# Kernel optimization log

Measured on AMD Instinct MI355X. Metric: run time of the kernel, lower is better.

Reference implementation:

```python
import jax, jax.numpy as jnp
import numpy as np

N, D, H, E, K = 16384, 256, 512, 16, 2  # nodes, node_dim, expert hidden, n_experts, active_k
LB_WEIGHT = 0.01
EPS = 1e-5


def setup_inputs() -> dict:
    key = jax.random.key(0)
    k0, k1, k2, k3 = jax.random.split(key, 4)
    x = jax.random.normal(k0, (N, D), jnp.float32)
    # router weight: torch nn.Linear(D, E, bias=False) -> weight [E, D], init std=0.02
    Wr = jax.random.normal(k1, (E, D), jnp.float32) * 0.02
    # stacked expert weights (torch Linear weights transposed to [in, out])
    W1 = jax.random.normal(k2, (E, D, H), jnp.float32) * 0.02
    W2 = jax.random.normal(k3, (E, H, D), jnp.float32) * 0.02
    ln_gamma = jnp.ones((D,), jnp.float32)
    ln_beta = jnp.zeros((D,), jnp.float32)
    return {"x": x, "Wr": Wr, "W1": W1, "W2": W2, "ln_gamma": ln_gamma, "ln_beta": ln_beta}


def reference(x, Wr, W1, W2, ln_gamma, ln_beta):
    n = x.shape[0]
    router_logits = x @ Wr.T                                  # [N, E]
    router_probs = jax.nn.softmax(router_logits, axis=-1)     # [N, E]
    top_w, top_i = jax.lax.top_k(router_probs, K)             # [N, K] each
    top_w = top_w / (top_w.sum(axis=-1, keepdims=True) + 1e-9)
    # dense combine weights: cw[n, e] = renormalized weight if e selected else 0
    cw = jnp.zeros((n, E), x.dtype).at[jnp.arange(n)[:, None], top_i].set(top_w)
    # per-expert FFN on all tokens (fixed-shape dense dispatch), exact-erf GELU like nn.GELU
    h = jax.nn.gelu(jnp.einsum('nd,edh->neh', x, W1), approximate=False)  # [N, E, H]
    y = jnp.einsum('neh,ehd->ned', h, W2)                     # [N, E, D]
    moe_out = jnp.einsum('ne,ned->nd', cw, y)                 # [N, D]
    # residual + LayerNorm
    z = x + moe_out
    mu = z.mean(axis=-1, keepdims=True)
    var = ((z - mu) ** 2).mean(axis=-1, keepdims=True)
    out = (z - mu) / jnp.sqrt(var + EPS) * ln_gamma + ln_beta
    # load-balance loss (counts are non-differentiable, like torch.no_grad())
    counts = jax.ops.segment_sum(jnp.ones((n * K,), router_probs.dtype),
                                 top_i.reshape(-1), num_segments=E)
    frac_tokens = jax.lax.stop_gradient(counts) / (n * K + 1e-9)
    lb_loss = LB_WEIGHT * (E * jnp.sum(frac_tokens * router_probs.mean(axis=0)))
    return out, lb_loss, jax.lax.stop_gradient(router_probs), top_i
```

## Files before the change

### kernel.cpp

```cpp
#include <hip/hip_runtime.h>
#include <hip/hip_bf16.h>
#include <math.h>

#define N_TOK 16384
#define DIM   256
#define HID   512
#define NEXP  16
#define NSLOT (N_TOK * 2)
#define RT    64
#define MAXT  (NSLOT / RT + NEXP)
#define XCDC  (MAXT / 8)

typedef __attribute__((ext_vector_type(8))) short bf16x8;
typedef __attribute__((ext_vector_type(4))) float f32x4;
#define MFMA(a, b, c) __builtin_amdgcn_mfma_f32_16x16x32_bf16(a, b, c, 0, 0, 0)

__device__ __forceinline__ unsigned short f2b(float f) {
  union { float f; unsigned int i; } c; c.f = f;
  unsigned int r = c.i + 0x7FFFu + ((c.i >> 16) & 1u);
  return (unsigned short)(r >> 16);
}

__device__ __forceinline__ float gelu_f(float v) {
  float v2 = v * v;
  float u2 = v * fmaf(0.10294322f, v2, 2.3022082f);
  float s  = __builtin_amdgcn_exp2f(u2);
  float r  = __builtin_amdgcn_rcpf(1.0f + s);
  return fmaf(-v, r, v);
}

__global__ __launch_bounds__(256) void prep_kernel(
    const float* __restrict__ W1, const float* __restrict__ W2,
    unsigned short* __restrict__ W1f, unsigned short* __restrict__ W2f)
{
  int id = blockIdx.x * 256 + threadIdx.x;
  if (id < 524288) {
    int i4 = id * 4;
    int inner = i4 & 31;
    int h  = (i4 >> 5) & 511;
    int kb = (i4 >> 14) & 7;
    int e  = i4 >> 17;
    const float* src = W1 + ((size_t)(e * 256 + kb * 32 + inner) * 512 + h);
    ushort4 o;
    o.x = f2b(src[0]); o.y = f2b(src[512]); o.z = f2b(src[1024]); o.w = f2b(src[1536]);
    *(ushort4*)(W1f + i4) = o;
  } else {
    int i4 = (id - 524288) * 4;
    int inner = i4 & 31;
    int d2 = (i4 >> 5) & 255;
    int kb = (i4 >> 13) & 15;
    int e  = i4 >> 17;
    const float* src = W2 + ((size_t)(e * 512 + kb * 32 + inner) * 256 + d2);
    ushort4 o;
    o.x = f2b(src[0]); o.y = f2b(src[256]); o.z = f2b(src[512]); o.w = f2b(src[768]);
    *(ushort4*)(W2f + i4) = o;
  }
}

__global__ __launch_bounds__(256) void router_kernel(
    const float* __restrict__ x, const float* __restrict__ Wr,
    float* __restrict__ probs_out, float* __restrict__ topi_out,
    float* __restrict__ topw, int* __restrict__ sel, float* __restrict__ g_partial,
    unsigned short* __restrict__ xb)
{
  __shared__ float sp[16];
  int tid = threadIdx.x;
  int wv = tid >> 6, lane = tid & 63;
  int tok = blockIdx.x * 4 + wv;
  int e = lane & 15, q = lane >> 4;
  if (tid < 16) sp[tid] = 0.f;
  __syncthreads();

  const float4* xr = (const float4*)(x + (size_t)tok * DIM + q * 64);
  const float4* wr = (const float4*)(Wr + (size_t)e * DIM + q * 64);
  float a0 = 0.f, a1 = 0.f, a2 = 0.f, a3 = 0.f;
  #pragma unroll
  for (int i = 0; i < 16; ++i) {
    float4 xa = xr[i], wa = wr[i];
    a0 += xa.x * wa.x; a1 += xa.y * wa.y; a2 += xa.z * wa.z; a3 += xa.w * wa.w;
  }
  float lg = (a0 + a1) + (a2 + a3);
  lg += __shfl_xor(lg, 16, 64);
  lg += __shfl_xor(lg, 32, 64);

  float mx = lg;
  #pragma unroll
  for (int o = 1; o < 16; o <<= 1) mx = fmaxf(mx, __shfl_xor(mx, o, 64));
  float ex = expf(lg - mx);
  float ssum = ex;
  #pragma unroll
  for (int o = 1; o < 16; o <<= 1) ssum += __shfl_xor(ssum, o, 64);
  float p = ex / ssum;

  if (lane < 16) {
    probs_out[(size_t)tok * NEXP + e] = p;
    atomicAdd(&sp[e], p);
  }

  {
    float4 xc = *(const float4*)(x + (size_t)tok * DIM + lane * 4);
    ushort4 o;
    o.x = f2b(xc.x); o.y = f2b(xc.y); o.z = f2b(xc.z); o.w = f2b(xc.w);
    *(ushort4*)(xb + (size_t)tok * DIM + lane * 4) = o;
  }

  float p1 = p; int i1 = e;
  #pragma unroll
  for (int o = 1; o < 16; o <<= 1) {
    float po = __shfl_xor(p1, o, 64); int io = __shfl_xor(i1, o, 64);
    if (po > p1 || (po == p1 && io < i1)) { p1 = po; i1 = io; }
  }
  float pm = (e == i1) ? -1.f : p;
  float p2 = pm; int i2 = e;
  #pragma unroll
  for (int o = 1; o < 16; o <<= 1) {
    float po = __shfl_xor(p2, o, 64); int io = __shfl_xor(i2, o, 64);
    if (po > p2 || (po == p2 && io < i2)) { p2 = po; i2 = io; }
  }
  if (lane == 0) {
    float rs = 1.0f / (p1 + p2 + 1e-9f);
    int s0 = tok * 2;
    topw[s0] = p1 * rs;  topw[s0 + 1] = p2 * rs;
    sel[s0] = i1;        sel[s0 + 1] = i2;
    topi_out[s0] = (float)i1;  topi_out[s0 + 1] = (float)i2;
  }
  __syncthreads();
  if (tid < 16) g_partial[(size_t)tid * 4096 + blockIdx.x] = sp[tid];
}

__global__ __launch_bounds__(256) void scatter_kernel(
    const int* __restrict__ sel, const float* __restrict__ topw,
    const float* __restrict__ g_partial,
    int* __restrict__ cursors, int* __restrict__ gdone,
    int* __restrict__ tok_of_pos, float* __restrict__ w_of_pos,
    float* __restrict__ zbuf, int* __restrict__ perm, float* __restrict__ lb_out)
{
  __shared__ int bcnt[16];
  __shared__ int bbase[16];
  int tid = threadIdx.x;
  if (tid < 16) bcnt[tid] = 0;
  __syncthreads();
  int s = blockIdx.x * 256 + tid;
  int e = sel[s];
  int my = atomicAdd(&bcnt[e], 1);
  __syncthreads();
  if (tid < 16) bbase[tid] = atomicAdd(&cursors[tid], bcnt[tid]);
  __syncthreads();
  int idx = e * NSLOT + bbase[e] + my;
  tok_of_pos[idx] = s >> 1;
  w_of_pos[idx]   = topw[s];

  {
    float4 zz = {0.f, 0.f, 0.f, 0.f};
    float4* zp = (float4*)zbuf + (size_t)blockIdx.x * 8192 + tid;
    #pragma unroll
    for (int i = 0; i < 32; ++i) zp[i * 256] = zz;
  }

  __threadfence();
  __shared__ int lastS;
  if (tid == 0) lastS = (atomicAdd(gdone, 1) == 127) ? 1 : 0;
  __syncthreads();
  if (!lastS) return;

  __shared__ float sp[16];
  __shared__ int nt[16];
  __shared__ int P[9];
  __shared__ int ccnt[16];
  int wv = tid >> 6, lane = tid & 63;
  if (tid < 16) ccnt[tid] = atomicAdd(&cursors[tid], 0);
  #pragma unroll
  for (int ee = 0; ee < 4; ++ee) {
    int ex = wv * 4 + ee;
    float sacc = 0.f;
    #pragma unroll
    for (int j = 0; j < 64; ++j) sacc += g_partial[(size_t)ex * 4096 + j * 64 + lane];
    #pragma unroll
    for (int o = 32; o; o >>= 1) sacc += __shfl_xor(sacc, o, 64);
    if (lane == 0) sp[ex] = sacc;
  }
  __syncthreads();
  if (tid < 16) nt[tid] = (ccnt[tid] + RT - 1) / RT;
  __syncthreads();
  if (tid == 0) {
    float acc = 0.f;
    for (int e2 = 0; e2 < NEXP; ++e2)
      acc += ((float)ccnt[e2] / (32768.0f + 1e-9f)) * (sp[e2] * (1.0f / 16384.0f));
    lb_out[0] = 0.01f * 16.0f * acc;
    int pp = 0;
    for (int g = 0; g < 8; ++g) { P[g] = pp; pp += nt[g] + nt[g + 8]; }
    P[8] = pp;
  }
  __syncthreads();
  for (int t = tid; t < MAXT; t += 256) {
    int g = 0;
    #pragma unroll
    for (int gg = 1; gg < 8; ++gg) if (t >= P[gg]) g = gg;
    int v = -1;
    if (t < P[8]) {
      int r = t - P[g];
      int e2 = (r < nt[g]) ? g : g + 8;
      int mt = (r < nt[g]) ? r : r - nt[g];
      v = (e2 << 16) | mt;
    }
    perm[t] = v;
  }
}

__global__ __launch_bounds__(512, 1) void ffn_kernel(
    const unsigned short* __restrict__ xb,
    const unsigned short* __restrict__ W1f, const unsigned short* __restrict__ W2f,
    const int* __restrict__ cursors, const int* __restrict__ perm,
    const int* __restrict__ tok_of_pos, const float* __restrict__ w_of_pos,
    float* __restrict__ zbuf)
{
  __shared__ __align__(16) unsigned short As[8 * 64 * 32];
  __shared__ __align__(16) unsigned short Hs[16 * 64 * 32];
  __shared__ float rwS[RT];
  __shared__ int   tokS[RT];

  int b = blockIdx.x;
  int rr = (b & 7) * XCDC + (b >> 3);
  int pv = perm[rr];
  if (pv < 0) return;
  int e = pv >> 16, mtile = pv & 0xFFFF;
  int cnt = cursors[e];
  int base = e * NSLOT;
  int m0 = mtile * RT;

  int tid = threadIdx.x;
  if (tid < RT) {
    int rl = m0 + tid;
    tokS[tid] = (rl < cnt) ? tok_of_pos[base + rl] : -1;
    rwS[tid]  = (rl < cnt) ? w_of_pos[base + rl] : 0.f;
  }
  __syncthreads();

  #pragma unroll
  for (int q = 0; q < 4; ++q) {
    int idx = q * 512 + tid;
    int row = idx >> 5, cb = idx & 31;
    int tk = tokS[row];
    bf16x8 v = {0, 0, 0, 0, 0, 0, 0, 0};
    if (tk >= 0) v = *(const bf16x8*)(xb + (size_t)tk * DIM + cb * 8);
    int si = ((cb >> 2) * 2048 + row * 32 + (cb & 3) * 8) ^ ((row & 7) << 3);
    *(bf16x8*)&As[si] = v;
  }
  __syncthreads();

  int lane = tid & 63;
  int w = tid >> 6;
  int l15 = lane & 15, g = lane >> 4;

  bf16x8 af[4][8];
  #pragma unroll
  for (int mf = 0; mf < 4; ++mf) {
    int row = mf * 16 + l15;
    #pragma unroll
    for (int kb = 0; kb < 8; ++kb)
      af[mf][kb] = *(const bf16x8*)&As[(kb * 2048 + row * 32 + g * 8) ^ ((row & 7) << 3)];
  }

  const unsigned short* W1e = W1f + (size_t)e * (8 * 512 * 32);
  #pragma unroll
  for (int cf = 0; cf < 4; ++cf) {
    int col0 = w * 64 + cf * 16;
    f32x4 ac[4];
    #pragma unroll
    for (int mf = 0; mf < 4; ++mf) ac[mf] = (f32x4){0.f, 0.f, 0.f, 0.f};
    #pragma unroll
    for (int kb = 0; kb < 8; ++kb) {
      bf16x8 bfr = *(const bf16x8*)(W1e + (size_t)(kb * 512 + col0 + l15) * 32 + g * 8);
      #pragma unroll
      for (int mf = 0; mf < 4; ++mf) ac[mf] = MFMA(af[mf][kb], bfr, ac[mf]);
    }
    int col = col0 + l15;
    #pragma unroll
    for (int mf = 0; mf < 4; ++mf) {
      #pragma unroll
      for (int reg = 0; reg < 4; ++reg) {
        int row = mf * 16 + g * 4 + reg;
        int si = ((col >> 5) * 2048 + row * 32 + (col & 31)) ^ ((row & 7) << 3);
        Hs[si] = f2b(gelu_f(ac[mf][reg]));
      }
    }
  }
  __syncthreads();

  const unsigned short* W2e = W2f + (size_t)e * (16 * 256 * 32);
  bf16x8 b2[2][16];
  #pragma unroll
  for (int cf = 0; cf < 2; ++cf)
    #pragma unroll
    for (int kb = 0; kb < 16; ++kb)
      b2[cf][kb] = *(const bf16x8*)(W2e + (size_t)(kb * 256 + w * 32 + cf * 16 + l15) * 32 + g * 8);

  #pragma unroll
  for (int mf = 0; mf < 4; ++mf) {
    f32x4 ac0 = {0.f, 0.f, 0.f, 0.f}, ac1 = {0.f, 0.f, 0.f, 0.f};
    int rowa = mf * 16 + l15;
    #pragma unroll
    for (int kb = 0; kb < 16; ++kb) {
      bf16x8 hfr = *(const bf16x8*)&Hs[(kb * 2048 + rowa * 32 + g * 8) ^ ((rowa & 7) << 3)];
      ac0 = MFMA(hfr, b2[0][kb], ac0);
      ac1 = MFMA(hfr, b2[1][kb], ac1);
    }
    #pragma unroll
    for (int reg = 0; reg < 4; ++reg) {
      int row = mf * 16 + g * 4 + reg;
      int t = tokS[row];
      if (t >= 0) {
        float rw = rwS[row];
        atomicAdd(zbuf + (size_t)t * DIM + w * 32 + l15,      ac0[reg] * rw);
        atomicAdd(zbuf + (size_t)t * DIM + w * 32 + 16 + l15, ac1[reg] * rw);
      }
    }
  }
}

__global__ __launch_bounds__(256) void combine_ln_kernel(
    const float* __restrict__ x, const float* __restrict__ zbuf,
    const float* __restrict__ gamma, const float* __restrict__ beta,
    float* __restrict__ outp)
{
  int wv = threadIdx.x >> 6, lane = threadIdx.x & 63;
  int tok = blockIdx.x * 4 + wv;
  int d0 = lane << 2;
  float4 xv = *(const float4*)(x + (size_t)tok * DIM + d0);
  float4 mv = *(const float4*)(zbuf + (size_t)tok * DIM + d0);
  float z0 = xv.x + mv.x, z1 = xv.y + mv.y, z2 = xv.z + mv.z, z3 = xv.w + mv.w;
  float s = z0 + z1 + z2 + z3;
  float q = z0 * z0 + z1 * z1 + z2 * z2 + z3 * z3;
  #pragma unroll
  for (int off = 32; off > 0; off >>= 1) {
    s += __shfl_xor(s, off, 64);
    q += __shfl_xor(q, off, 64);
  }
  float mu  = s * (1.0f / 256.0f);
  float var = q * (1.0f / 256.0f) - mu * mu;
  float inv = rsqrtf(var + 1e-5f);
  float4 gv = *(const float4*)(gamma + d0);
  float4 bv = *(const float4*)(beta + d0);
  float4 ov;
  ov.x = (z0 - mu) * inv * gv.x + bv.x;
  ov.y = (z1 - mu) * inv * gv.y + bv.y;
  ov.z = (z2 - mu) * inv * gv.z + bv.z;
  ov.w = (z3 - mu) * inv * gv.w + bv.w;
  *(float4*)(outp + (size_t)tok * DIM + d0) = ov;
}

extern "C" void kernel_launch(void* const* d_in, const int* in_sizes, int n_in,
                              void* d_out, int out_size, void* d_ws, size_t ws_size,
                              hipStream_t stream)
{
  const float* x     = (const float*)d_in[0];
  const float* Wr    = (const float*)d_in[1];
  const float* W1    = (const float*)d_in[2];
  const float* W2    = (const float*)d_in[3];
  const float* gamma = (const float*)d_in[4];
  const float* beta  = (const float*)d_in[5];

  float* ob = (float*)d_out;
  float* out_main  = ob;
  float* lb_out    = ob + (size_t)N_TOK * DIM;
  float* probs_out = ob + (size_t)N_TOK * DIM + 1;
  float* topi_out  = ob + (size_t)N_TOK * DIM + 1 + (size_t)N_TOK * NEXP;

  char* ws = (char*)d_ws;
  int*   cursors    = (int*)(ws + 0);
  int*   gdone      = (int*)(ws + 64);
  int*   perm       = (int*)(ws + 1024);
  float* g_partial  = (float*)(ws + 65536);
  float* topw       = (float*)(ws + 327680);
  int*   sel        = (int*)(ws + 458752);
  int*   tok_of_pos = (int*)(ws + 589824);
  float* w_of_pos   = (float*)(ws + 2686976);
  unsigned short* xb  = (unsigned short*)(ws + 4980736);
  unsigned short* W1f = (unsigned short*)(ws + 13369344);
  unsigned short* W2f = (unsigned short*)(ws + 17563648);
  float* zbuf       = (float*)(ws + 21757952);

  hipMemsetAsync(cursors, 0, 128, stream);
  prep_kernel<<<4096, 256, 0, stream>>>(W1, W2, W1f, W2f);
  router_kernel<<<N_TOK / 4, 256, 0, stream>>>(x, Wr, probs_out, topi_out, topw, sel, g_partial, xb);
  scatter_kernel<<<NSLOT / 256, 256, 0, stream>>>(sel, topw, g_partial, cursors, gdone,
                                                  tok_of_pos, w_of_pos, zbuf, perm, lb_out);
  ffn_kernel<<<MAXT, 512, 0, stream>>>(xb, W1f, W2f, cursors, perm, tok_of_pos, w_of_pos, zbuf);
  combine_ln_kernel<<<N_TOK / 4, 256, 0, stream>>>(x, zbuf, gamma, beta, out_main);
}
```

Baseline: 225.9 us.

## Replace atomic zbuf accumulation with per-slot bf16 outputs and fuse prep with router

Each expert-slot result is written as bf16 into a per-slot buffer that the LayerNorm kernel sums, instead of fp32 atomics into a zeroed zbuf. This removes the zbuf zeroing in scatter and the atomic traffic. The FFN kernel moves to 256 threads with 2 blocks per CU and processes the hidden dimension in two phases with a smaller H tile in LDS, accumulating the second GEMM in registers. The weight prep and router kernels are merged into one launch. The cost is bf16 rounding of the partial outputs and some repeated W1/W2 fragment loads.

```diff
diff --git a/kernel.cpp b/kernel.cpp
--- a/kernel.cpp
+++ b/kernel.cpp
@@ -29,44 +29,45 @@
   return fmaf(-v, r, v);
 }
 
-__global__ __launch_bounds__(256) void prep_kernel(
+__global__ __launch_bounds__(256) void prep_router_kernel(
     const float* __restrict__ W1, const float* __restrict__ W2,
-    unsigned short* __restrict__ W1f, unsigned short* __restrict__ W2f)
-{
-  int id = blockIdx.x * 256 + threadIdx.x;
-  if (id < 524288) {
-    int i4 = id * 4;
-    int inner = i4 & 31;
-    int h  = (i4 >> 5) & 511;
-    int kb = (i4 >> 14) & 7;
-    int e  = i4 >> 17;
-    const float* src = W1 + ((size_t)(e * 256 + kb * 32 + inner) * 512 + h);
-    ushort4 o;
-    o.x = f2b(src[0]); o.y = f2b(src[512]); o.z = f2b(src[1024]); o.w = f2b(src[1536]);
-    *(ushort4*)(W1f + i4) = o;
-  } else {
-    int i4 = (id - 524288) * 4;
-    int inner = i4 & 31;
-    int d2 = (i4 >> 5) & 255;
-    int kb = (i4 >> 13) & 15;
-    int e  = i4 >> 17;
-    const float* src = W2 + ((size_t)(e * 512 + kb * 32 + inner) * 256 + d2);
-    ushort4 o;
-    o.x = f2b(src[0]); o.y = f2b(src[256]); o.z = f2b(src[512]); o.w = f2b(src[768]);
-    *(ushort4*)(W2f + i4) = o;
-  }
-}
-
-__global__ __launch_bounds__(256) void router_kernel(
     const float* __restrict__ x, const float* __restrict__ Wr,
+    unsigned short* __restrict__ W1f, unsigned short* __restrict__ W2f,
     float* __restrict__ probs_out, float* __restrict__ topi_out,
     float* __restrict__ topw, int* __restrict__ sel, float* __restrict__ g_partial,
     unsigned short* __restrict__ xb)
 {
+  if (blockIdx.x < 4096) {
+    int id = blockIdx.x * 256 + threadIdx.x;
+    if (id < 524288) {
+      int i4 = id * 4;
+      int inner = i4 & 31;
+      int h  = (i4 >> 5) & 511;
+      int kb = (i4 >> 14) & 7;
+      int e  = i4 >> 17;
+      const float* src = W1 + ((size_t)(e * 256 + kb * 32 + inner) * 512 + h);
+      ushort4 o;
+      o.x = f2b(src[0]); o.y = f2b(src[512]); o.z = f2b(src[1024]); o.w = f2b(src[1536]);
+      *(ushort4*)(W1f + i4) = o;
+    } else {
+      int i4 = (id - 524288) * 4;
+      int inner = i4 & 31;
+      int d2 = (i4 >> 5) & 255;
+      int kb = (i4 >> 13) & 15;
+      int e  = i4 >> 17;
+      const float* src = W2 + ((size_t)(e * 512 + kb * 32 + inner) * 256 + d2);
+      ushort4 o;
+      o.x = f2b(src[0]); o.y = f2b(src[256]); o.z = f2b(src[512]); o.w = f2b(src[768]);
+      *(ushort4*)(W2f + i4) = o;
+    }
+    return;
+  }
+
   __shared__ float sp[16];
+  int bid = blockIdx.x - 4096;
   int tid = threadIdx.x;
   int wv = tid >> 6, lane = tid & 63;
-  int tok = blockIdx.x * 4 + wv;
+  int tok = bid * 4 + wv;
   int e = lane & 15, q = lane >> 4;
   if (tid < 16) sp[tid] = 0.f;
   __syncthreads();
@@ -125,15 +126,15 @@
     topi_out[s0] = (float)i1;  topi_out[s0 + 1] = (float)i2;
   }
   __syncthreads();
-  if (tid < 16) g_partial[(size_t)tid * 4096 + blockIdx.x] = sp[tid];
+  if (tid < 16) g_partial[(size_t)tid * 4096 + bid] = sp[tid];
 }
 
 __global__ __launch_bounds__(256) void scatter_kernel(
     const int* __restrict__ sel, const float* __restrict__ topw,
     const float* __restrict__ g_partial,
     int* __restrict__ cursors, int* __restrict__ gdone,
-    int* __restrict__ tok_of_pos, float* __restrict__ w_of_pos,
-    float* __restrict__ zbuf, int* __restrict__ perm, float* __restrict__ lb_out)
+    int* __restrict__ slotA, float* __restrict__ w_of_pos,
+    int* __restrict__ perm, float* __restrict__ lb_out)
 {
   __shared__ int bcnt[16];
   __shared__ int bbase[16];
@@ -147,15 +148,8 @@
   if (tid < 16) bbase[tid] = atomicAdd(&cursors[tid], bcnt[tid]);
   __syncthreads();
   int idx = e * NSLOT + bbase[e] + my;
-  tok_of_pos[idx] = s >> 1;
-  w_of_pos[idx]   = topw[s];
-
-  {
-    float4 zz = {0.f, 0.f, 0.f, 0.f};
-    float4* zp = (float4*)zbuf + (size_t)blockIdx.x * 8192 + tid;
-    #pragma unroll
-    for (int i = 0; i < 32; ++i) zp[i * 256] = zz;
-  }
+  slotA[idx]    = s;
+  w_of_pos[idx] = topw[s];
 
   __threadfence();
   __shared__ int lastS;
@@ -207,17 +201,17 @@
   }
 }
 
-__global__ __launch_bounds__(512, 1) void ffn_kernel(
+__global__ __launch_bounds__(256, 2) void ffn_kernel(
     const unsigned short* __restrict__ xb,
     const unsigned short* __restrict__ W1f, const unsigned short* __restrict__ W2f,
     const int* __restrict__ cursors, const int* __restrict__ perm,
-    const int* __restrict__ tok_of_pos, const float* __restrict__ w_of_pos,
-    float* __restrict__ zbuf)
+    const int* __restrict__ slotA, const float* __restrict__ w_of_pos,
+    unsigned short* __restrict__ ybuf)
 {
   __shared__ __align__(16) unsigned short As[8 * 64 * 32];
-  __shared__ __align__(16) unsigned short Hs[16 * 64 * 32];
+  __shared__ __align__(16) unsigned short Hs[8 * 64 * 32];
   __shared__ float rwS[RT];
-  __shared__ int   tokS[RT];
+  __shared__ int   slotS[RT];
 
   int b = blockIdx.x;
   int rr = (b & 7) * XCDC + (b >> 3);
@@ -231,18 +225,18 @@
   int tid = threadIdx.x;
   if (tid < RT) {
     int rl = m0 + tid;
-    tokS[tid] = (rl < cnt) ? tok_of_pos[base + rl] : -1;
-    rwS[tid]  = (rl < cnt) ? w_of_pos[base + rl] : 0.f;
-  }
-  __syncthreads();
-
-  #pragma unroll
-  for (int q = 0; q < 4; ++q) {
-    int idx = q * 512 + tid;
+    slotS[tid] = (rl < cnt) ? slotA[base + rl] : -1;
+    rwS[tid]   = (rl < cnt) ? w_of_pos[base + rl] : 0.f;
+  }
+  __syncthreads();
+
+  #pragma unroll
+  for (int q = 0; q < 8; ++q) {
+    int idx = q * 256 + tid;
     int row = idx >> 5, cb = idx & 31;
-    int tk = tokS[row];
+    int s = slotS[row];
     bf16x8 v = {0, 0, 0, 0, 0, 0, 0, 0};
-    if (tk >= 0) v = *(const bf16x8*)(xb + (size_t)tk * DIM + cb * 8);
+    if (s >= 0) v = *(const bf16x8*)(xb + (size_t)(s >> 1) * DIM + cb * 8);
     int si = ((cb >> 2) * 2048 + row * 32 + (cb & 3) * 8) ^ ((row & 7) << 3);
     *(bf16x8*)&As[si] = v;
   }
@@ -261,65 +255,80 @@
       af[mf][kb] = *(const bf16x8*)&As[(kb * 2048 + row * 32 + g * 8) ^ ((row & 7) << 3)];
   }
 
+  f32x4 acY[4][4];
+  #pragma unroll
+  for (int cf = 0; cf < 4; ++cf)
+    #pragma unroll
+    for (int mf = 0; mf < 4; ++mf) acY[cf][mf] = (f32x4){0.f, 0.f, 0.f, 0.f};
+
   const unsigned short* W1e = W1f + (size_t)e * (8 * 512 * 32);
-  #pragma unroll
-  for (int cf = 0; cf < 4; ++cf) {
-    int col0 = w * 64 + cf * 16;
-    f32x4 ac[4];
-    #pragma unroll
-    for (int mf = 0; mf < 4; ++mf) ac[mf] = (f32x4){0.f, 0.f, 0.f, 0.f};
-    #pragma unroll
-    for (int kb = 0; kb < 8; ++kb) {
-      bf16x8 bfr = *(const bf16x8*)(W1e + (size_t)(kb * 512 + col0 + l15) * 32 + g * 8);
+  const unsigned short* W2e = W2f + (size_t)e * (16 * 256 * 32);
+
+  #pragma unroll
+  for (int ph = 0; ph < 2; ++ph) {
+    #pragma unroll
+    for (int cf = 0; cf < 4; ++cf) {
+      int col = ph * 256 + w * 64 + cf * 16;
+      f32x4 ac[4];
       #pragma unroll
-      for (int mf = 0; mf < 4; ++mf) ac[mf] = MFMA(af[mf][kb], bfr, ac[mf]);
-    }
-    int col = col0 + l15;
-    #pragma unroll
-    for (int mf = 0; mf < 4; ++mf) {
+      for (int mf = 0; mf < 4; ++mf) ac[mf] = (f32x4){0.f, 0.f, 0.f, 0.f};
       #pragma unroll
-      for (int reg = 0; reg < 4; ++reg) {
-        int row = mf * 16 + g * 4 + reg;
-        int si = ((col >> 5) * 2048 + row * 32 + (col & 31)) ^ ((row & 7) << 3);
-        Hs[si] = f2b(gelu_f(ac[mf][reg]));
+      for (int kb = 0; kb < 8; ++kb) {
+        bf16x8 bfr = *(const bf16x8*)(W1e + (size_t)(kb * 512 + col + l15) * 32 + g * 8);
+        #pragma unroll
+        for (int mf = 0; mf < 4; ++mf) ac[mf] = MFMA(af[mf][kb], bfr, ac[mf]);
+      }
+      int colL = w * 64 + cf * 16 + l15;
+      #pragma unroll
+      for (int mf = 0; mf < 4; ++mf) {
+        #pragma unroll
+        for (int reg = 0; reg < 4; ++reg) {
+          int row = mf * 16 + g * 4 + reg;
+          int si = ((colL >> 5) * 2048 + row * 32 + (colL & 31)) ^ ((row & 7) << 3);
+          Hs[si] = f2b(gelu_f(ac[mf][reg]));
+        }
       }
     }
-  }
-  __syncthreads();
-
-  const unsigned short* W2e = W2f + (size_t)e * (16 * 256 * 32);
-  bf16x8 b2[2][16];
-  #pragma unroll
-  for (int cf = 0; cf < 2; ++cf)
-    #pragma unroll
-    for (int kb = 0; kb < 16; ++kb)
-      b2[cf][kb] = *(const bf16x8*)(W2e + (size_t)(kb * 256 + w * 32 + cf * 16 + l15) * 32 + g * 8);
+    __syncthreads();
+
+    #pragma unroll
+    for (int kbL = 0; kbL < 8; ++kbL) {
+      int kb = ph * 8 + kbL;
+      bf16x8 hfr[4];
+      #pragma unroll
+      for (int mf = 0; mf < 4; ++mf) {
+        int row = mf * 16 + l15;
+        hfr[mf] = *(const bf16x8*)&Hs[(kbL * 2048 + row * 32 + g * 8) ^ ((row & 7) << 3)];
+      }
+      #pragma unroll
+      for (int cf = 0; cf < 4; ++cf) {
+        bf16x8 b2 = *(const bf16x8*)(W2e + (size_t)(kb * 256 + w * 64 + cf * 16 + l15) * 32 + g * 8);
+        #pragma unroll
+        for (int mf = 0; mf < 4; ++mf) acY[cf][mf] = MFMA(hfr[mf], b2, acY[cf][mf]);
+      }
+    }
+    if (ph == 0) __syncthreads();
+  }
 
   #pragma unroll
   for (int mf = 0; mf < 4; ++mf) {
-    f32x4 ac0 = {0.f, 0.f, 0.f, 0.f}, ac1 = {0.f, 0.f, 0.f, 0.f};
-    int rowa = mf * 16 + l15;
-    #pragma unroll
-    for (int kb = 0; kb < 16; ++kb) {
-      bf16x8 hfr = *(const bf16x8*)&Hs[(kb * 2048 + rowa * 32 + g * 8) ^ ((rowa & 7) << 3)];
-      ac0 = MFMA(hfr, b2[0][kb], ac0);
-      ac1 = MFMA(hfr, b2[1][kb], ac1);
-    }
     #pragma unroll
     for (int reg = 0; reg < 4; ++reg) {
       int row = mf * 16 + g * 4 + reg;
-      int t = tokS[row];
-      if (t >= 0) {
+      int s = slotS[row];
+      if (s >= 0) {
         float rw = rwS[row];
-        atomicAdd(zbuf + (size_t)t * DIM + w * 32 + l15,      ac0[reg] * rw);
-        atomicAdd(zbuf + (size_t)t * DIM + w * 32 + 16 + l15, ac1[reg] * rw);
+        unsigned short* yp = ybuf + (size_t)s * DIM + w * 64 + l15;
+        #pragma unroll
+        for (int cf = 0; cf < 4; ++cf)
+          yp[cf * 16] = f2b(acY[cf][mf][reg] * rw);
       }
     }
   }
 }
 
 __global__ __launch_bounds__(256) void combine_ln_kernel(
-    const float* __restrict__ x, const float* __restrict__ zbuf,
+    const float* __restrict__ x, const unsigned short* __restrict__ ybuf,
     const float* __restrict__ gamma, const float* __restrict__ beta,
     float* __restrict__ outp)
 {
@@ -327,8 +336,17 @@
   int tok = blockIdx.x * 4 + wv;
   int d0 = lane << 2;
   float4 xv = *(const float4*)(x + (size_t)tok * DIM + d0);
-  float4 mv = *(const float4*)(zbuf + (size_t)tok * DIM + d0);
-  float z0 = xv.x + mv.x, z1 = xv.y + mv.y, z2 = xv.z + mv.z, z3 = xv.w + mv.w;
+  ushort4 u0 = *(const ushort4*)(ybuf + (size_t)(tok * 2) * DIM + d0);
+  ushort4 u1 = *(const ushort4*)(ybuf + (size_t)(tok * 2 + 1) * DIM + d0);
+  union { unsigned int i; float f; } c0, c1, c2, c3, d1, d2_, d3, d4;
+  c0.i = (unsigned int)u0.x << 16; c1.i = (unsigned int)u0.y << 16;
+  c2.i = (unsigned int)u0.z << 16; c3.i = (unsigned int)u0.w << 16;
+  d1.i = (unsigned int)u1.x << 16; d2_.i = (unsigned int)u1.y << 16;
+  d3.i = (unsigned int)u1.z << 16; d4.i = (unsigned int)u1.w << 16;
+  float z0 = xv.x + c0.f + d1.f;
+  float z1 = xv.y + c1.f + d2_.f;
+  float z2 = xv.z + c2.f + d3.f;
+  float z3 = xv.w + c3.f + d4.f;
   float s = z0 + z1 + z2 + z3;
   float q = z0 * z0 + z1 * z1 + z2 * z2 + z3 * z3;
   #pragma unroll
@@ -373,18 +391,18 @@
   float* g_partial  = (float*)(ws + 65536);
   float* topw       = (float*)(ws + 327680);
   int*   sel        = (int*)(ws + 458752);
-  int*   tok_of_pos = (int*)(ws + 589824);
+  int*   slotA      = (int*)(ws + 589824);
   float* w_of_pos   = (float*)(ws + 2686976);
   unsigned short* xb  = (unsigned short*)(ws + 4980736);
   unsigned short* W1f = (unsigned short*)(ws + 13369344);
   unsigned short* W2f = (unsigned short*)(ws + 17563648);
-  float* zbuf       = (float*)(ws + 21757952);
+  unsigned short* ybuf = (unsigned short*)(ws + 21757952);
 
   hipMemsetAsync(cursors, 0, 128, stream);
-  prep_kernel<<<4096, 256, 0, stream>>>(W1, W2, W1f, W2f);
-  router_kernel<<<N_TOK / 4, 256, 0, stream>>>(x, Wr, probs_out, topi_out, topw, sel, g_partial, xb);
+  prep_router_kernel<<<8192, 256, 0, stream>>>(W1, W2, x, Wr, W1f, W2f,
+                                               probs_out, topi_out, topw, sel, g_partial, xb);
   scatter_kernel<<<NSLOT / 256, 256, 0, stream>>>(sel, topw, g_partial, cursors, gdone,
-                                                  tok_of_pos, w_of_pos, zbuf, perm, lb_out);
-  ffn_kernel<<<MAXT, 512, 0, stream>>>(xb, W1f, W2f, cursors, perm, tok_of_pos, w_of_pos, zbuf);
-  combine_ln_kernel<<<N_TOK / 4, 256, 0, stream>>>(x, zbuf, gamma, beta, out_main);
-}
+                                                  slotA, w_of_pos, perm, lb_out);
+  ffn_kernel<<<MAXT, 256, 0, stream>>>(xb, W1f, W2f, cursors, perm, slotA, w_of_pos, ybuf);
+  combine_ln_kernel<<<N_TOK / 4, 256, 0, stream>>>(x, ybuf, gamma, beta, out_main);
+}
```

New measurement: 273.6 us. +21.1%, slower.
